# Optimization experiments

Hardware: AMD Instinct MI355X
Metric: run time of the kernel (lower is better)

## Reference

```python
import jax, jax.numpy as jnp
import numpy as np

TAU = 2.0      # LIF membrane time constant
VTH = 1.0      # spike threshold
ALPHA = 2.0    # surrogate-gradient sharpness (atan surrogate)
EPS = 1e-5     # BatchNorm eps

@jax.custom_vjp
def spike(u):
    return (u > 0.0).astype(u.dtype)

def _spike_fwd(u):
    return spike(u), u

def _spike_bwd(u, g):
    sg = ALPHA / (2.0 * (1.0 + (jnp.pi / 2.0 * ALPHA * u) ** 2))
    return (g * sg,)

spike.defvjp(_spike_fwd, _spike_bwd)

def lif_time(x):
    # x: [B,T,C,H,W] -> spikes [B,T,C,H,W]; hard-reset LIF, v0 = 0
    xT = jnp.moveaxis(x, 1, 0)  # [T,B,C,H,W]
    def step(v, xt):
        v = v + (xt - v) / TAU
        s = spike(v - VTH)
        return v * (1.0 - s), s
    _, sT = jax.lax.scan(step, jnp.zeros_like(xT[0]), xT)
    return jnp.moveaxis(sT, 0, 1)

def conv2d(x, w, stride, pad):
    return jax.lax.conv_general_dilated(
        x, w, (stride, stride), [(pad, pad), (pad, pad)],
        dimension_numbers=('NCHW', 'OIHW', 'NCHW'))

def bn(x, gamma, beta, mean, var):
    # inference-style BatchNorm2d with running stats; x: [N,C,H,W]
    inv = gamma * jax.lax.rsqrt(var + EPS)
    return x * inv[None, :, None, None] + (beta - mean * inv)[None, :, None, None]

def setup_inputs() -> dict:
    key = jax.random.key(0)
    ks = jax.random.split(key, 16)
    B, T, Cin, Cout, H, W = 16, 8, 128, 256, 56, 56
    d = {}
    d['x_spike'] = (jax.random.uniform(ks[0], (B, T, Cin, H, W)) < 0.2).astype(jnp.float32)
    d['conv1_w'] = jax.random.normal(ks[1], (Cout, Cin, 3, 3), dtype=jnp.float32) * 0.05
    d['conv2_w'] = jax.random.normal(ks[2], (Cout, Cout, 3, 3), dtype=jnp.float32) * 0.05
    d['ds_w'] = jax.random.normal(ks[3], (Cout, Cin, 1, 1), dtype=jnp.float32) * 0.05
    for i, p in enumerate(['n1', 'n2', 'nd']):
        d[p + '_gamma'] = 1.0 + 0.1 * jax.random.normal(ks[4 + i], (Cout,), dtype=jnp.float32)
        d[p + '_beta'] = 0.1 * jax.random.normal(ks[7 + i], (Cout,), dtype=jnp.float32)
        d[p + '_mean'] = 0.01 * jax.random.normal(ks[10 + i], (Cout,), dtype=jnp.float32)
        d[p + '_var'] = jax.random.uniform(ks[13 + i], (Cout,), minval=0.5, maxval=1.5)
    return d

def reference(x_spike, conv1_w, conv2_w, ds_w,
              n1_gamma, n1_beta, n1_mean, n1_var,
              n2_gamma, n2_beta, n2_mean, n2_var,
              nd_gamma, nd_beta, nd_mean, nd_var):
    B, T, Cin, H, W = x_spike.shape
    x_flat = x_spike.reshape(B * T, Cin, H, W)
    # downsample shortcut (1x1 conv stride 2 + BN)
    identity = bn(conv2d(x_flat, ds_w, 2, 0), nd_gamma, nd_beta, nd_mean, nd_var)
    # NOTE: original module runs lif_shortcut on identity but DISCARDS the result
    # (pure state side-effect); it does not affect the output, so it is omitted.
    out = bn(conv2d(x_flat, conv1_w, 2, 1), n1_gamma, n1_beta, n1_mean, n1_var)
    Cout, Ho, Wo = out.shape[1], out.shape[2], out.shape[3]
    out = lif_time(out.reshape(B, T, Cout, Ho, Wo))
    out = bn(conv2d(out.reshape(B * T, Cout, Ho, Wo), conv2_w, 1, 1),
             n2_gamma, n2_beta, n2_mean, n2_var) + identity
    return lif_time(out.reshape(B, T, Cout, Ho, Wo))
```

## Files before the change

### kernel.cpp

```cpp
#include <hip/hip_runtime.h>
#include <hip/hip_bf16.h>

#define CIN  128
#define CO   256
#define HIN  56
#define WIN  56
#define OH   28
#define OWW  28
#define P    784
#define HWIN 3136
#define PERT 200704

typedef __attribute__((ext_vector_type(8))) short bf16x8v;
typedef __attribute__((ext_vector_type(4))) float f32x4;

__device__ __forceinline__ f32x4 mfma16(bf16x8v a, bf16x8v b, f32x4 c) {
    return __builtin_amdgcn_mfma_f32_16x16x32_bf16(a, b, c, 0, 0, 0);
}

__device__ __forceinline__ void gld_lds16(const void* g, void* l) {
    __builtin_amdgcn_global_load_lds(
        (const __attribute__((address_space(1))) void*)g,
        (__attribute__((address_space(3))) void*)l, 16, 0, 0);
}

__global__ __launch_bounds__(256) void k_prep_bias(
    const float* __restrict__ g1, const float* __restrict__ b1,
    const float* __restrict__ m1, const float* __restrict__ v1,
    const float* __restrict__ g2, const float* __restrict__ b2,
    const float* __restrict__ m2, const float* __restrict__ v2,
    const float* __restrict__ gd, const float* __restrict__ bd,
    const float* __restrict__ md, const float* __restrict__ vd,
    float* __restrict__ inv1o, float* __restrict__ bias1o,
    float* __restrict__ inv2o, float* __restrict__ invdo,
    float* __restrict__ bias2o)
{
    int co = threadIdx.x;
    float inv1 = g1[co] / sqrtf(v1[co] + 1e-5f);
    float inv2 = g2[co] / sqrtf(v2[co] + 1e-5f);
    float invd = gd[co] / sqrtf(vd[co] + 1e-5f);
    inv1o[co]  = inv1;
    bias1o[co] = fmaf(-m1[co], inv1, b1[co]);
    inv2o[co]  = inv2;
    invdo[co]  = invd;
    bias2o[co] = fmaf(-m2[co], inv2, b2[co]) + fmaf(-md[co], invd, bd[co]);
}

__global__ __launch_bounds__(256) void k_prep_w2p(
    const float* __restrict__ w2, const float* __restrict__ inv2,
    unsigned short* __restrict__ hi, unsigned short* __restrict__ lo)
{
    int i = blockIdx.x * 256 + threadIdx.x;
    if (i >= 73728) return;
    int tap = i >> 13;
    int r   = i & 8191;
    int ch  = r >> 10;
    int r2  = r & 1023;
    int cf  = r2 >> 6;
    int lane = r2 & 63;
    int co  = cf * 16 + (lane & 15);
    int cib = ch * 32 + (lane >> 4) * 8;
#pragma unroll
    for (int j = 0; j < 8; j++) {
        float w = w2[((size_t)co * CO + cib + j) * 9 + tap] * inv2[co];
        __hip_bfloat16 h = __float2bfloat16(w);
        __hip_bfloat16 l = __float2bfloat16(w - __bfloat162float(h));
        hi[(size_t)i * 8 + j] = *(unsigned short*)&h;
        lo[(size_t)i * 8 + j] = *(unsigned short*)&l;
    }
}

__global__ __launch_bounds__(256) void k_prep_w1p(
    const float* __restrict__ w1, const float* __restrict__ inv1,
    unsigned short* __restrict__ hi, unsigned short* __restrict__ mid,
    unsigned short* __restrict__ lo)
{
    int i = blockIdx.x * 256 + threadIdx.x;
    if (i >= 36864) return;
    int tap = i >> 12;
    int r   = i & 4095;
    int ch  = r >> 10;
    int r2  = r & 1023;
    int cf  = r2 >> 6;
    int lane = r2 & 63;
    int co  = cf * 16 + (lane & 15);
    int cib = ch * 32 + (lane >> 4) * 8;
#pragma unroll
    for (int j = 0; j < 8; j++) {
        float w = w1[((size_t)co * CIN + cib + j) * 9 + tap] * inv1[co];
        __hip_bfloat16 h = __float2bfloat16(w);
        float r1 = w - __bfloat162float(h);
        __hip_bfloat16 m = __float2bfloat16(r1);
        float r2f = r1 - __bfloat162float(m);
        __hip_bfloat16 l = __float2bfloat16(r2f);
        hi[(size_t)i * 8 + j]  = *(unsigned short*)&h;
        mid[(size_t)i * 8 + j] = *(unsigned short*)&m;
        lo[(size_t)i * 8 + j]  = *(unsigned short*)&l;
    }
}

__global__ __launch_bounds__(256) void k_prep_wdp(
    const float* __restrict__ wd, const float* __restrict__ invd,
    unsigned short* __restrict__ hi, unsigned short* __restrict__ lo)
{
    int i = blockIdx.x * 256 + threadIdx.x;
    if (i >= 4096) return;
    int ch  = i >> 10;
    int r2  = i & 1023;
    int cf  = r2 >> 6;
    int lane = r2 & 63;
    int co  = cf * 16 + (lane & 15);
    int cib = ch * 32 + (lane >> 4) * 8;
#pragma unroll
    for (int j = 0; j < 8; j++) {
        float w = wd[(size_t)co * CIN + cib + j] * invd[co];
        __hip_bfloat16 h = __float2bfloat16(w);
        __hip_bfloat16 l = __float2bfloat16(w - __bfloat162float(h));
        hi[(size_t)i * 8 + j] = *(unsigned short*)&h;
        lo[(size_t)i * 8 + j] = *(unsigned short*)&l;
    }
}

__global__ __launch_bounds__(256) void k_pack1(
    const float* __restrict__ x, unsigned int* __restrict__ xt_p)
{
    int i = blockIdx.x * 256 + threadIdx.x;
    int pos = i % HWIN;
    int nw  = i / HWIN;
    int w   = nw & 3;
    int n   = nw >> 2;
    const float* xp = x + ((size_t)n * CIN + w * 32) * HWIN + pos;
    unsigned int word = 0;
#pragma unroll
    for (int ci = 0; ci < 32; ci++)
        if (xp[(size_t)ci * HWIN] != 0.f) word |= (1u << ci);
    xt_p[((size_t)n * HWIN + pos) * 4 + w] = word;
}

__global__ __launch_bounds__(256) void k_conv1_mfma(
    const unsigned int* __restrict__ xt_p,
    const unsigned short* __restrict__ w1hip,
    const unsigned short* __restrict__ w1midp,
    const unsigned short* __restrict__ w1lop,
    const float* __restrict__ bias1,
    float* __restrict__ out)
{
    __shared__ unsigned int XW[4 * 522];

    const int n    = blockIdx.x / 7;
    const int rt   = blockIdx.x - n * 7;
    const int r0   = rt * 4;
    const int tid  = threadIdx.x;
    const int wave = tid >> 6;
    const int lane = tid & 63;
    const int l15  = lane & 15;
    const int quad = lane >> 4;
    const int cf0  = wave * 4;

    const unsigned int* xp_n = xt_p + (size_t)n * HWIN * 4;
    for (int i = tid; i < 513; i += 256) {
        int row = i / 57, c = i - row * 57;
        int irow = 2 * r0 - 1 + row;
        int iw   = c - 1;
        uint4 val = {0u, 0u, 0u, 0u};
        if (irow >= 0 && iw >= 0)
            val = *(const uint4*)(xp_n + (size_t)(irow * WIN + iw) * 4);
        int base = row * 58 + c;
        XW[0 * 522 + base] = val.x;
        XW[1 * 522 + base] = val.y;
        XW[2 * 522 + base] = val.z;
        XW[3 * 522 + base] = val.w;
    }
    __syncthreads();

    int rr[7], cc[7];
#pragma unroll
    for (int f = 0; f < 7; f++) {
        int pos = f * 16 + l15;
        rr[f] = pos / 28;
        cc[f] = pos - rr[f] * 28;
    }

    f32x4 acc[4][7];
#pragma unroll
    for (int g = 0; g < 4; g++)
#pragma unroll
        for (int f = 0; f < 7; f++) acc[g][f] = (f32x4){0.f, 0.f, 0.f, 0.f};

    for (int c = 0; c < 4; c++) {
        for (int tap = 0; tap < 9; tap++) {
            size_t b0 = ((size_t)(tap * 4 + c) * 16 + cf0) * 512 + lane * 8;
            bf16x8v ah[4], am[4], al[4];
#pragma unroll
            for (int g = 0; g < 4; g++) {
                ah[g] = *(const bf16x8v*)(w1hip  + b0 + g * 512);
                am[g] = *(const bf16x8v*)(w1midp + b0 + g * 512);
                al[g] = *(const bf16x8v*)(w1lop  + b0 + g * 512);
            }
            const int kh = tap / 3, kw = tap - kh * 3;
#pragma unroll
            for (int f = 0; f < 7; f++) {
                unsigned int word = XW[c * 522 + (2 * rr[f] + kh) * 58 + 2 * cc[f] + kw];
                unsigned int byt  = (word >> (quad * 8)) & 0xffu;
                uint4 u;
                u.x = ((byt & 1u)   ? 0x3F80u : 0u) | ((byt & 2u)   ? 0x3F800000u : 0u);
                u.y = ((byt & 4u)   ? 0x3F80u : 0u) | ((byt & 8u)   ? 0x3F800000u : 0u);
                u.z = ((byt & 16u)  ? 0x3F80u : 0u) | ((byt & 32u)  ? 0x3F800000u : 0u);
                u.w = ((byt & 64u)  ? 0x3F80u : 0u) | ((byt & 128u) ? 0x3F800000u : 0u);
                union { uint4 q; bf16x8v v; } cv;
                cv.q = u;
#pragma unroll
                for (int g = 0; g < 4; g++) {
                    acc[g][f] = mfma16(ah[g], cv.v, acc[g][f]);
                    acc[g][f] = mfma16(am[g], cv.v, acc[g][f]);
                    acc[g][f] = mfma16(al[g], cv.v, acc[g][f]);
                }
            }
        }
    }

#pragma unroll
    for (int g = 0; g < 4; g++)
#pragma unroll
        for (int f = 0; f < 7; f++) {
            int pg = rt * 112 + f * 16 + l15;
#pragma unroll
            for (int reg = 0; reg < 4; reg++) {
                int co = (cf0 + g) * 16 + quad * 4 + reg;
                out[((size_t)n * CO + co) * P + pg] = acc[g][f][reg] + bias1[co];
            }
        }
}

__global__ __launch_bounds__(256) void k_lif1t(
    const float* __restrict__ pre, unsigned short* __restrict__ st)
{
    __shared__ unsigned short T[16 * 68];
    const int b   = blockIdx.x;
    const int co0 = blockIdx.y * 64;
    const int p0  = blockIdx.z * 16;
    const int tid  = threadIdx.x;
    const int pcol = tid & 15;
    const int g    = tid >> 4;
    const int pos = p0 + g;
    const int oh  = pos / 28, ow = pos - oh * 28;
    const int f8  = ((((oh + 1) * 30 + ow + 1) >> 1) & 3);
    const int o      = (pcol & 7) >> 1;
    const int no     = o ^ f8;
    const int within = (pcol & 1) * 4;
    const int chp    = (co0 >> 5) + (pcol >> 3);
    float v[4] = {0.f, 0.f, 0.f, 0.f};
    for (int t = 0; t < 8; t++) {
        const float* src = pre + (((size_t)(b * 8 + t)) * CO + co0) * P + p0;
        unsigned short s[4];
#pragma unroll
        for (int j = 0; j < 4; j++) {
            int co = g + 16 * j;
            float xv = src[(size_t)co * P + pcol];
            v[j] = v[j] + (xv - v[j]) * 0.5f;
            bool sp = v[j] > 1.0f;
            s[j] = sp ? 0x3F80 : 0;
            if (sp) v[j] = 0.f;
        }
        __syncthreads();
#pragma unroll
        for (int j = 0; j < 4; j++) T[pcol * 68 + g + 16 * j] = s[j];
        __syncthreads();
        unsigned short* dst = st + (((size_t)(b * 8 + t) * 8 + chp) * P + pos) * 32
                               + no * 8 + within;
        ushort4 ov;
        ov.x = T[g * 68 + pcol * 4 + 0];
        ov.y = T[g * 68 + pcol * 4 + 1];
        ov.z = T[g * 68 + pcol * 4 + 2];
        ov.w = T[g * 68 + pcol * 4 + 3];
        *(ushort4*)dst = ov;
    }
}

__global__ __launch_bounds__(256) void k_conv2_mfma(
    const unsigned short* __restrict__ spike_t,
    const unsigned int* __restrict__ xt_p,
    const unsigned short* __restrict__ w2hip,
    const unsigned short* __restrict__ w2lop,
    const unsigned short* __restrict__ wdhip,
    const unsigned short* __restrict__ wdlop,
    const float* __restrict__ bias2,
    float* __restrict__ out)
{
    __shared__ unsigned short SB[2 * 5760];
    __shared__ unsigned int   XW2[4 * 112];

    const int n    = blockIdx.x / 7;
    const int rt   = blockIdx.x - n * 7;
    const int r0   = rt * 4;
    const int tid  = threadIdx.x;
    const int wave = tid >> 6;
    const int lane = tid & 63;
    const int l15  = lane & 15;
    const int quad = lane >> 4;
    const int cf0  = wave * 4;

    {
        uint4 z = {0u, 0u, 0u, 0u};
        for (int i = tid; i < 1440; i += 256) ((uint4*)SB)[i] = z;
    }
    for (int i = tid; i < 112; i += 256) {
        int r = i / 28, c = i - r * 28;
        uint4 w4 = *(const uint4*)(xt_p + ((size_t)n * HWIN
                    + (2 * (r0 + r)) * WIN + 2 * c) * 4);
        XW2[0 * 112 + i] = w4.x;
        XW2[1 * 112 + i] = w4.y;
        XW2[2 * 112 + i] = w4.z;
        XW2[3 * 112 + i] = w4.w;
    }
    __syncthreads();

    int  g_irow[3], g_lds[3];
    bool g_ok[3];
    int  g_half[3];
#pragma unroll
    for (int k = 0; k < 3; k++) {
        int idx  = wave * 3 + k;
        int row  = idx >> 1, half = idx & 1;
        int irow = r0 - 1 + row;
        g_irow[k] = irow;
        g_half[k] = half;
        g_ok[k]   = ((unsigned)irow < 28u) && (half == 0 || lane < 48);
        g_lds[k]  = row * 1920 + 64 + half * 1024;
    }
    const char* sp_n = (const char*)spike_t + (size_t)n * 8 * P * 64;

#pragma unroll
    for (int k = 0; k < 3; k++)
        if (g_ok[k])
            gld_lds16(sp_n + (size_t)g_irow[k] * 1792 + g_half[k] * 1024 + lane * 16,
                      (char*)SB + g_lds[k]);

    int rr[7], cc[7];
#pragma unroll
    for (int f = 0; f < 7; f++) {
        int pos = f * 16 + l15;
        rr[f] = pos / 28;
        cc[f] = pos - rr[f] * 28;
    }

    f32x4 acc[4][7];
#pragma unroll
    for (int g = 0; g < 4; g++)
#pragma unroll
        for (int f = 0; f < 7; f++) acc[g][f] = (f32x4){0.f, 0.f, 0.f, 0.f};

    for (int c = 0; c < 4; c++) {
        size_t b0 = ((size_t)c * 16 + cf0) * 512 + lane * 8;
        bf16x8v ah[4], al[4];
#pragma unroll
        for (int g = 0; g < 4; g++) {
            ah[g] = *(const bf16x8v*)(wdhip + b0 + g * 512);
            al[g] = *(const bf16x8v*)(wdlop + b0 + g * 512);
        }
#pragma unroll
        for (int f = 0; f < 7; f++) {
            unsigned int word = XW2[c * 112 + rr[f] * 28 + cc[f]];
            unsigned int byt  = (word >> (quad * 8)) & 0xffu;
            uint4 u;
            u.x = ((byt & 1u)   ? 0x3F80u : 0u) | ((byt & 2u)   ? 0x3F800000u : 0u);
            u.y = ((byt & 4u)   ? 0x3F80u : 0u) | ((byt & 8u)   ? 0x3F800000u : 0u);
            u.z = ((byt & 16u)  ? 0x3F80u : 0u) | ((byt & 32u)  ? 0x3F800000u : 0u);
            u.w = ((byt & 64u)  ? 0x3F80u : 0u) | ((byt & 128u) ? 0x3F800000u : 0u);
            union { uint4 q; bf16x8v v; } cv;
            cv.q = u;
#pragma unroll
            for (int g = 0; g < 4; g++) {
                acc[g][f] = mfma16(ah[g], cv.v, acc[g][f]);
                acc[g][f] = mfma16(al[g], cv.v, acc[g][f]);
            }
        }
    }
    __syncthreads();

    bf16x8v cw[8], nx[8];
    {
        size_t b0 = ((size_t)0 * 16 + cf0) * 512 + lane * 8;
#pragma unroll
        for (int g = 0; g < 4; g++) {
            cw[2 * g]     = *(const bf16x8v*)(w2hip + b0 + g * 512);
            cw[2 * g + 1] = *(const bf16x8v*)(w2lop + b0 + g * 512);
            nx[2 * g]     = cw[2 * g];
            nx[2 * g + 1] = cw[2 * g + 1];
        }
    }

    for (int c = 0; c < 8; c++) {
        if (c < 7) {
            const char* base = sp_n + (size_t)(c + 1) * 50176;
            char* dstb = (char*)SB + ((c + 1) & 1) * 11520;
#pragma unroll
            for (int k = 0; k < 3; k++)
                if (g_ok[k])
                    gld_lds16(base + (size_t)g_irow[k] * 1792 + g_half[k] * 1024 + lane * 16,
                              dstb + g_lds[k]);
        }
        const int bufsh = (c & 1) * 5760;
        for (int tap = 0; tap < 9; tap++) {
            int rd = c * 9 + tap;
            if (rd < 71) {
                int rn = rd + 1, cn = rn / 9, tn = rn - cn * 9;
                size_t b0 = ((size_t)(tn * 8 + cn) * 16 + cf0) * 512 + lane * 8;
#pragma unroll
                for (int g = 0; g < 4; g++) {
                    nx[2 * g]     = *(const bf16x8v*)(w2hip + b0 + g * 512);
                    nx[2 * g + 1] = *(const bf16x8v*)(w2lop + b0 + g * 512);
                }
            }
            const int kh = tap / 3, kw = tap - kh * 3;
#pragma unroll
            for (int f = 0; f < 7; f++) {
                int slot = (rr[f] + kh) * 30 + cc[f] + kw;
                int sw   = (slot >> 1) & 3;
                bf16x8v bfr = *(const bf16x8v*)(
                    &SB[bufsh + slot * 32 + ((quad ^ sw) * 8)]);
#pragma unroll
                for (int g = 0; g < 4; g++) {
                    acc[g][f] = mfma16(cw[2 * g], bfr, acc[g][f]);
                    acc[g][f] = mfma16(cw[2 * g + 1], bfr, acc[g][f]);
                }
            }
#pragma unroll
            for (int j = 0; j < 8; j++) cw[j] = nx[j];
        }
        __syncthreads();
    }

#pragma unroll
    for (int g = 0; g < 4; g++)
#pragma unroll
        for (int f = 0; f < 7; f++) {
            int pg = rt * 112 + f * 16 + l15;
#pragma unroll
            for (int reg = 0; reg < 4; reg++) {
                int co = (cf0 + g) * 16 + quad * 4 + reg;
                out[((size_t)n * CO + co) * P + pg] = acc[g][f][reg] + bias2[co];
            }
        }
}

__global__ __launch_bounds__(256) void k_lif4(const float4* __restrict__ in,
                                              float4* __restrict__ out)
{
    const int q = PERT / 4;
    const int i = blockIdx.x * 256 + threadIdx.x;
    const int b = i / q;
    const int r = i - b * q;
    const float4* pi = in  + (size_t)(b * 8) * q + r;
    float4*       po = out + (size_t)(b * 8) * q + r;
    float v0 = 0.f, v1 = 0.f, v2 = 0.f, v3 = 0.f;
#pragma unroll
    for (int t = 0; t < 8; t++) {
        float4 xt = pi[(size_t)t * q];
        float4 s;
        v0 = v0 + (xt.x - v0) * 0.5f; s.x = (v0 > 1.0f) ? 1.f : 0.f; if (v0 > 1.0f) v0 = 0.f;
        v1 = v1 + (xt.y - v1) * 0.5f; s.y = (v1 > 1.0f) ? 1.f : 0.f; if (v1 > 1.0f) v1 = 0.f;
        v2 = v2 + (xt.z - v2) * 0.5f; s.z = (v2 > 1.0f) ? 1.f : 0.f; if (v2 > 1.0f) v2 = 0.f;
        v3 = v3 + (xt.w - v3) * 0.5f; s.w = (v3 > 1.0f) ? 1.f : 0.f; if (v3 > 1.0f) v3 = 0.f;
        po[(size_t)t * q] = s;
    }
}

extern "C" void kernel_launch(void* const* d_in, const int* in_sizes, int n_in,
                              void* d_out, int out_size, void* d_ws, size_t ws_size,
                              hipStream_t stream) {
    const float* x   = (const float*)d_in[0];
    const float* w1  = (const float*)d_in[1];
    const float* w2  = (const float*)d_in[2];
    const float* wd  = (const float*)d_in[3];
    const float* n1g = (const float*)d_in[4];
    const float* n1b = (const float*)d_in[5];
    const float* n1m = (const float*)d_in[6];
    const float* n1v = (const float*)d_in[7];
    const float* n2g = (const float*)d_in[8];
    const float* n2b = (const float*)d_in[9];
    const float* n2m = (const float*)d_in[10];
    const float* n2v = (const float*)d_in[11];
    const float* ndg = (const float*)d_in[12];
    const float* ndb = (const float*)d_in[13];
    const float* ndm = (const float*)d_in[14];
    const float* ndv = (const float*)d_in[15];

    float* out = (float*)d_out;

    char* w = (char*)d_ws;
    unsigned short* spike_t = (unsigned short*)w;
    unsigned short* w2hip   = (unsigned short*)(w + 51380224);
    unsigned short* w2lop   = (unsigned short*)(w + 52559872);
    unsigned short* w1hip   = (unsigned short*)(w + 53739520);
    unsigned short* w1midp  = (unsigned short*)(w + 54329344);
    unsigned short* w1lop   = (unsigned short*)(w + 54919168);
    unsigned short* wdhip   = (unsigned short*)(w + 55508992);
    unsigned short* wdlop   = (unsigned short*)(w + 55574528);
    float*          bias2   = (float*)(w + 55640064);
    float*          bias1   = (float*)(w + 55641088);
    float*          inv1    = (float*)(w + 55642112);
    float*          inv2    = (float*)(w + 55643136);
    float*          invd    = (float*)(w + 55644160);
    unsigned int*   xt_p    = (unsigned int*)(w + 55645184);

    k_prep_bias<<<1, 256, 0, stream>>>(n1g, n1b, n1m, n1v,
                                       n2g, n2b, n2m, n2v,
                                       ndg, ndb, ndm, ndv,
                                       inv1, bias1, inv2, invd, bias2);
    k_prep_w2p<<<288, 256, 0, stream>>>(w2, inv2, w2hip, w2lop);
    k_prep_w1p<<<144, 256, 0, stream>>>(w1, inv1, w1hip, w1midp, w1lop);
    k_prep_wdp<<<16, 256, 0, stream>>>(wd, invd, wdhip, wdlop);

    k_pack1<<<(128 * 4 * HWIN) / 256, 256, 0, stream>>>(x, xt_p);
    k_conv1_mfma<<<dim3(896), 256, 0, stream>>>(
        xt_p, w1hip, w1midp, w1lop, bias1, out);
    k_lif1t<<<dim3(16, 4, 49), 256, 0, stream>>>(out, spike_t);
    k_conv2_mfma<<<dim3(896), 256, 0, stream>>>(
        spike_t, xt_p, w2hip, w2lop, wdhip, wdlop, bias2, out);
    k_lif4<<<(16 * (PERT / 4)) / 256, 256, 0, stream>>>(
        (const float4*)out, (float4*)out);
}
```

Measured before the change: 722.2 us.

## Bit-pack LIF1 spikes and expand them in-register inside conv2

The first LIF stage now emits spikes as 32-bit bitmasks (one bit per channel) instead of bf16 swizzled tiles, cutting the spike intermediate from about 51 MB to about 3 MB. Conv2 loads all eight channel-chunks of a 6x30 halo into LDS once at the start and expands each byte into bf16 ones and zeros per tap before the MFMAs, the same way the shortcut path already does. This removes the double-buffered async global-to-LDS pipeline and its per-chunk barriers. The cost is extra ALU work for bit expansion in the inner loop, and a LIF kernel that runs far fewer blocks, each looping over 64 channels serially.

```diff
diff --git a/kernel.cpp b/kernel.cpp
--- a/kernel.cpp
+++ b/kernel.cpp
@@ -16,12 +16,6 @@
 
 __device__ __forceinline__ f32x4 mfma16(bf16x8v a, bf16x8v b, f32x4 c) {
     return __builtin_amdgcn_mfma_f32_16x16x32_bf16(a, b, c, 0, 0, 0);
-}
-
-__device__ __forceinline__ void gld_lds16(const void* g, void* l) {
-    __builtin_amdgcn_global_load_lds(
-        (const __attribute__((address_space(1))) void*)g,
-        (__attribute__((address_space(3))) void*)l, 16, 0, 0);
 }
 
 __global__ __launch_bounds__(256) void k_prep_bias(
@@ -233,52 +227,44 @@
 }
 
 __global__ __launch_bounds__(256) void k_lif1t(
-    const float* __restrict__ pre, unsigned short* __restrict__ st)
-{
-    __shared__ unsigned short T[16 * 68];
-    const int b   = blockIdx.x;
-    const int co0 = blockIdx.y * 64;
-    const int p0  = blockIdx.z * 16;
-    const int tid  = threadIdx.x;
-    const int pcol = tid & 15;
-    const int g    = tid >> 4;
-    const int pos = p0 + g;
-    const int oh  = pos / 28, ow = pos - oh * 28;
-    const int f8  = ((((oh + 1) * 30 + ow + 1) >> 1) & 3);
-    const int o      = (pcol & 7) >> 1;
-    const int no     = o ^ f8;
-    const int within = (pcol & 1) * 4;
-    const int chp    = (co0 >> 5) + (pcol >> 3);
-    float v[4] = {0.f, 0.f, 0.f, 0.f};
-    for (int t = 0; t < 8; t++) {
-        const float* src = pre + (((size_t)(b * 8 + t)) * CO + co0) * P + p0;
-        unsigned short s[4];
-#pragma unroll
-        for (int j = 0; j < 4; j++) {
-            int co = g + 16 * j;
-            float xv = src[(size_t)co * P + pcol];
-            v[j] = v[j] + (xv - v[j]) * 0.5f;
-            bool sp = v[j] > 1.0f;
-            s[j] = sp ? 0x3F80 : 0;
-            if (sp) v[j] = 0.f;
-        }
-        __syncthreads();
-#pragma unroll
-        for (int j = 0; j < 4; j++) T[pcol * 68 + g + 16 * j] = s[j];
-        __syncthreads();
-        unsigned short* dst = st + (((size_t)(b * 8 + t) * 8 + chp) * P + pos) * 32
-                               + no * 8 + within;
-        ushort4 ov;
-        ov.x = T[g * 68 + pcol * 4 + 0];
-        ov.y = T[g * 68 + pcol * 4 + 1];
-        ov.z = T[g * 68 + pcol * 4 + 2];
-        ov.w = T[g * 68 + pcol * 4 + 3];
-        *(ushort4*)dst = ov;
+    const float* __restrict__ pre, unsigned int* __restrict__ sp_p)
+{
+    const int b    = blockIdx.x;
+    const int z    = blockIdx.z;
+    const int wv   = threadIdx.x >> 6;
+    const int lane = threadIdx.x & 63;
+    const int pt   = blockIdx.y * 4 + wv;
+    const int pos  = pt * 64 + lane;
+    if (pos >= P) return;
+
+    unsigned int wb[8];
+#pragma unroll
+    for (int t = 0; t < 8; t++) wb[t] = 0u;
+    int widx = z * 2;
+
+    for (int cog = 0; cog < 64; cog++) {
+        const int co = z * 64 + cog;
+        const float* src = pre + ((size_t)(b * 8) * CO + co) * P + pos;
+        float v = 0.f;
+#pragma unroll
+        for (int t = 0; t < 8; t++) {
+            float xv = src[(size_t)t * CO * P];
+            v = v + (xv - v) * 0.5f;
+            if (v > 1.0f) { wb[t] |= (1u << (cog & 31)); v = 0.f; }
+        }
+        if ((cog & 31) == 31) {
+#pragma unroll
+            for (int t = 0; t < 8; t++) {
+                sp_p[((size_t)(b * 8 + t) * P + pos) * 8 + widx] = wb[t];
+                wb[t] = 0u;
+            }
+            widx++;
+        }
     }
 }
 
 __global__ __launch_bounds__(256) void k_conv2_mfma(
-    const unsigned short* __restrict__ spike_t,
+    const unsigned int* __restrict__ sp_p,
     const unsigned int* __restrict__ xt_p,
     const unsigned short* __restrict__ w2hip,
     const unsigned short* __restrict__ w2lop,
@@ -287,8 +273,8 @@
     const float* __restrict__ bias2,
     float* __restrict__ out)
 {
-    __shared__ unsigned short SB[2 * 5760];
-    __shared__ unsigned int   XW2[4 * 112];
+    __shared__ unsigned int SW[180 * 9];
+    __shared__ unsigned int XW2[4 * 112];
 
     const int n    = blockIdx.x / 7;
     const int rt   = blockIdx.x - n * 7;
@@ -300,9 +286,14 @@
     const int quad = lane >> 4;
     const int cf0  = wave * 4;
 
-    {
-        uint4 z = {0u, 0u, 0u, 0u};
-        for (int i = tid; i < 1440; i += 256) ((uint4*)SB)[i] = z;
+    for (int i = tid; i < 1440; i += 256) {
+        int slot = i >> 3, w = i & 7;
+        int row = slot / 30, col = slot - row * 30;
+        int irow = r0 - 1 + row, icol = col - 1;
+        unsigned int v = 0u;
+        if ((unsigned)irow < 28u && (unsigned)icol < 28u)
+            v = sp_p[((size_t)n * P + irow * 28 + icol) * 8 + w];
+        SW[slot * 9 + w] = v;
     }
     for (int i = tid; i < 112; i += 256) {
         int r = i / 28, c = i - r * 28;
@@ -314,27 +305,6 @@
         XW2[3 * 112 + i] = w4.w;
     }
     __syncthreads();
-
-    int  g_irow[3], g_lds[3];
-    bool g_ok[3];
-    int  g_half[3];
-#pragma unroll
-    for (int k = 0; k < 3; k++) {
-        int idx  = wave * 3 + k;
-        int row  = idx >> 1, half = idx & 1;
-        int irow = r0 - 1 + row;
-        g_irow[k] = irow;
-        g_half[k] = half;
-        g_ok[k]   = ((unsigned)irow < 28u) && (half == 0 || lane < 48);
-        g_lds[k]  = row * 1920 + 64 + half * 1024;
-    }
-    const char* sp_n = (const char*)spike_t + (size_t)n * 8 * P * 64;
-
-#pragma unroll
-    for (int k = 0; k < 3; k++)
-        if (g_ok[k])
-            gld_lds16(sp_n + (size_t)g_irow[k] * 1792 + g_half[k] * 1024 + lane * 16,
-                      (char*)SB + g_lds[k]);
 
     int rr[7], cc[7];
 #pragma unroll
@@ -376,7 +346,6 @@
             }
         }
     }
-    __syncthreads();
 
     bf16x8v cw[8], nx[8];
     {
@@ -391,16 +360,6 @@
     }
 
     for (int c = 0; c < 8; c++) {
-        if (c < 7) {
-            const char* base = sp_n + (size_t)(c + 1) * 50176;
-            char* dstb = (char*)SB + ((c + 1) & 1) * 11520;
-#pragma unroll
-            for (int k = 0; k < 3; k++)
-                if (g_ok[k])
-                    gld_lds16(base + (size_t)g_irow[k] * 1792 + g_half[k] * 1024 + lane * 16,
-                              dstb + g_lds[k]);
-        }
-        const int bufsh = (c & 1) * 5760;
         for (int tap = 0; tap < 9; tap++) {
             int rd = c * 9 + tap;
             if (rd < 71) {
@@ -416,19 +375,24 @@
 #pragma unroll
             for (int f = 0; f < 7; f++) {
                 int slot = (rr[f] + kh) * 30 + cc[f] + kw;
-                int sw   = (slot >> 1) & 3;
-                bf16x8v bfr = *(const bf16x8v*)(
-                    &SB[bufsh + slot * 32 + ((quad ^ sw) * 8)]);
+                unsigned int word = SW[slot * 9 + c];
+                unsigned int byt  = (word >> (quad * 8)) & 0xffu;
+                uint4 u;
+                u.x = ((byt & 1u)   ? 0x3F80u : 0u) | ((byt & 2u)   ? 0x3F800000u : 0u);
+                u.y = ((byt & 4u)   ? 0x3F80u : 0u) | ((byt & 8u)   ? 0x3F800000u : 0u);
+                u.z = ((byt & 16u)  ? 0x3F80u : 0u) | ((byt & 32u)  ? 0x3F800000u : 0u);
+                u.w = ((byt & 64u)  ? 0x3F80u : 0u) | ((byt & 128u) ? 0x3F800000u : 0u);
+                union { uint4 q; bf16x8v v; } cv;
+                cv.q = u;
 #pragma unroll
                 for (int g = 0; g < 4; g++) {
-                    acc[g][f] = mfma16(cw[2 * g], bfr, acc[g][f]);
-                    acc[g][f] = mfma16(cw[2 * g + 1], bfr, acc[g][f]);
+                    acc[g][f] = mfma16(cw[2 * g], cv.v, acc[g][f]);
+                    acc[g][f] = mfma16(cw[2 * g + 1], cv.v, acc[g][f]);
                 }
             }
 #pragma unroll
             for (int j = 0; j < 8; j++) cw[j] = nx[j];
         }
-        __syncthreads();
     }
 
 #pragma unroll
@@ -489,20 +453,20 @@
     float* out = (float*)d_out;
 
     char* w = (char*)d_ws;
-    unsigned short* spike_t = (unsigned short*)w;
-    unsigned short* w2hip   = (unsigned short*)(w + 51380224);
-    unsigned short* w2lop   = (unsigned short*)(w + 52559872);
-    unsigned short* w1hip   = (unsigned short*)(w + 53739520);
-    unsigned short* w1midp  = (unsigned short*)(w + 54329344);
-    unsigned short* w1lop   = (unsigned short*)(w + 54919168);
-    unsigned short* wdhip   = (unsigned short*)(w + 55508992);
-    unsigned short* wdlop   = (unsigned short*)(w + 55574528);
-    float*          bias2   = (float*)(w + 55640064);
-    float*          bias1   = (float*)(w + 55641088);
-    float*          inv1    = (float*)(w + 55642112);
-    float*          inv2    = (float*)(w + 55643136);
-    float*          invd    = (float*)(w + 55644160);
-    unsigned int*   xt_p    = (unsigned int*)(w + 55645184);
+    unsigned int*   sp_p    = (unsigned int*)w;
+    unsigned short* w2hip   = (unsigned short*)(w + 3211264);
+    unsigned short* w2lop   = (unsigned short*)(w + 4390912);
+    unsigned short* w1hip   = (unsigned short*)(w + 5570560);
+    unsigned short* w1midp  = (unsigned short*)(w + 6160384);
+    unsigned short* w1lop   = (unsigned short*)(w + 6750208);
+    unsigned short* wdhip   = (unsigned short*)(w + 7340032);
+    unsigned short* wdlop   = (unsigned short*)(w + 7405568);
+    float*          bias2   = (float*)(w + 7471104);
+    float*          bias1   = (float*)(w + 7472128);
+    float*          inv1    = (float*)(w + 7473152);
+    float*          inv2    = (float*)(w + 7474176);
+    float*          invd    = (float*)(w + 7475200);
+    unsigned int*   xt_p    = (unsigned int*)(w + 7476224);
 
     k_prep_bias<<<1, 256, 0, stream>>>(n1g, n1b, n1m, n1v,
                                        n2g, n2b, n2m, n2v,
@@ -515,9 +479,9 @@
     k_pack1<<<(128 * 4 * HWIN) / 256, 256, 0, stream>>>(x, xt_p);
     k_conv1_mfma<<<dim3(896), 256, 0, stream>>>(
         xt_p, w1hip, w1midp, w1lop, bias1, out);
-    k_lif1t<<<dim3(16, 4, 49), 256, 0, stream>>>(out, spike_t);
+    k_lif1t<<<dim3(16, 4, 4), 256, 0, stream>>>(out, sp_p);
     k_conv2_mfma<<<dim3(896), 256, 0, stream>>>(
-        spike_t, xt_p, w2hip, w2lop, wdhip, wdlop, bias2, out);
+        sp_p, xt_p, w2hip, w2lop, wdhip, wdlop, bias2, out);
     k_lif4<<<(16 * (PERT / 4)) / 256, 256, 0, stream>>>(
         (const float4*)out, (float4*)out);
 }
```

New measurement: 791.8 us. +9.6%, slower.
